# Performance work log

Measured on AMD Instinct MI355X. Metric: run time of the kernel, lower is better.

Reference implementation:

```python
import jax, jax.numpy as jnp
import numpy as np

B, T, D_IN, H, C = 16, 8192, 4, 256, 11


def setup_inputs() -> dict:
    key = jax.random.key(0)
    ks = jax.random.split(key, 9)
    sequence = jax.random.normal(ks[0], (B, T, D_IN), jnp.float32)
    # lengths in [7*T/8, T] so every sequence has mask[:,0]=True (torchcrf requirement)
    lengths = (T - jax.random.randint(ks[1], (B,), 0, T // 8)).astype(jnp.int64)
    labels = jax.random.randint(ks[2], (B, T), 0, C).astype(jnp.int64)
    W_enc = jax.random.normal(ks[3], (D_IN, H), jnp.float32) / np.float32(np.sqrt(D_IN))
    b_enc = jnp.zeros((H,), jnp.float32)
    W_emit = jax.random.normal(ks[4], (H, C), jnp.float32) / np.float32(np.sqrt(H))
    b_emit = jnp.zeros((C,), jnp.float32)
    start_trans = jax.random.normal(ks[5], (C,), jnp.float32) * 0.1
    trans = jax.random.normal(ks[6], (C, C), jnp.float32) * 0.1
    end_trans = jax.random.normal(ks[7], (C,), jnp.float32) * 0.1
    return dict(sequence=sequence, W_enc=W_enc, b_enc=b_enc, W_emit=W_emit,
                b_emit=b_emit, start_trans=start_trans, trans=trans,
                end_trans=end_trans, lengths=lengths, labels=labels)


def reference(sequence, W_enc, b_enc, W_emit, b_emit, start_trans, trans, end_trans, lengths, labels):
    # encoder (Linear + ReLU) and emission projection
    hidden = jax.nn.relu(sequence @ W_enc + b_enc)        # [B,T,H]
    em = hidden @ W_emit + b_emit                          # [B,T,C]
    mask = jnp.arange(T)[None, :] < lengths[:, None]       # [B,T] bool
    maskf = mask.astype(em.dtype)
    tags = jnp.where(labels == -100, 0, labels)            # -100 -> 0 as in compute_loss

    # ---- numerator: score of the gold path (torchcrf _compute_score) ----
    em_tag = jnp.take_along_axis(em, tags[..., None], axis=2)[..., 0]   # [B,T]
    trans_tag = trans[tags[:, :-1], tags[:, 1:]]                        # [B,T-1]
    num = start_trans[tags[:, 0]] + em_tag[:, 0]
    num = num + jnp.sum(maskf[:, 1:] * (trans_tag + em_tag[:, 1:]), axis=1)
    last_tag = tags[jnp.arange(B), lengths - 1]
    num = num + end_trans[last_tag]

    # ---- denominator: log partition via forward algorithm (torchcrf _compute_normalizer) ----
    alpha0 = start_trans[None, :] + em[:, 0]               # [B,C]
    em_rest = jnp.swapaxes(em[:, 1:], 0, 1)                # [T-1,B,C]
    mask_rest = jnp.swapaxes(mask[:, 1:], 0, 1)            # [T-1,B]

    def step(alpha, inp):
        em_t, m_t = inp
        nxt = jax.nn.logsumexp(alpha[:, :, None] + trans[None] + em_t[:, None, :], axis=1)
        return jnp.where(m_t[:, None], nxt, alpha), None

    alpha, _ = jax.lax.scan(step, alpha0, (em_rest, mask_rest))
    den = jax.nn.logsumexp(alpha + end_trans[None, :], axis=1)  # [B]

    # reduction='mean' over batch, loss = -log_likelihood
    return -jnp.mean(num - den)
```

## Files before the change

kernel.cpp:

```cpp
#include <hip/hip_runtime.h>
#include <hip/hip_bf16.h>

#define B_   16
#define T_   8192
#define H_   256
#define C_   11
#define KCH  256
#define LCH  32
#define NC   (B_*KCH)

typedef __attribute__((ext_vector_type(8))) short short8;
typedef __attribute__((ext_vector_type(4))) float f32x4;

__global__ __launch_bounds__(256) void k_em(
    const float* __restrict__ seq, const float* __restrict__ Wenc,
    const float* __restrict__ benc, const float* __restrict__ Wemit,
    const float* __restrict__ bemit, const float* __restrict__ trans,
    const float* __restrict__ startt, const float* __restrict__ endt,
    const int* __restrict__ lengths, const int* __restrict__ labels,
    unsigned short* __restrict__ expem, float* __restrict__ numpart,
    unsigned* __restrict__ counter)
{
    __shared__ float ldsWpack[2048];
    __shared__ float ldsWemit[4096];
    __shared__ float red[4];
    int tid = threadIdx.x;
    if (blockIdx.x == 0 && tid == 0) counter[0] = 0;

    for (int idx = tid; idx < 2048; idx += 256) {
        int h = idx >> 3, s = idx & 7;
        float v = 0.f;
        if (s < 4) v = Wenc[s * H_ + h];
        else if (s == 4) v = benc[h];
        ldsWpack[idx] = v;
    }
    for (int idx = tid; idx < 4096; idx += 256) {
        int h = idx >> 4, c = idx & 15;
        ldsWemit[idx] = (c < C_) ? Wemit[h * C_ + c] : 0.f;
    }
    __syncthreads();

    int wid = tid >> 6, lane = tid & 63;
    int g = lane >> 4, li = lane & 15;
    int b0 = blockIdx.x >> 5;
    int tb0 = (blockIdx.x & 31) * 256 + wid * 64;
    size_t grow0 = (size_t)b0 * T_ + tb0;

    float4 xs[4];
#pragma unroll
    for (int tt = 0; tt < 4; tt++)
        xs[tt] = *(const float4*)(seq + (grow0 + tt * 16 + li) * 4);

    f32x4 acc[4];
#pragma unroll
    for (int tt = 0; tt < 4; tt++) acc[tt] = (f32x4){0.f, 0.f, 0.f, 0.f};

#pragma unroll 1
    for (int kb = 0; kb < 8; kb++) {
        float We[8][5], wm[8];
#pragma unroll
        for (int e = 0; e < 8; e++) {
            int h = 32 * kb + 4 * g + (e & 3) + 16 * (e >> 2);
            float4 w4 = *(const float4*)&ldsWpack[h * 8];
            We[e][0] = w4.x; We[e][1] = w4.y; We[e][2] = w4.z; We[e][3] = w4.w;
            We[e][4] = ldsWpack[h * 8 + 4];
            wm[e] = ldsWemit[h * 16 + li];
        }
        unsigned a0, a1, a2, a3;
        asm("v_cvt_pk_bf16_f32 %0, %1, %2" : "=v"(a0) : "v"(wm[0]), "v"(wm[1]));
        asm("v_cvt_pk_bf16_f32 %0, %1, %2" : "=v"(a1) : "v"(wm[2]), "v"(wm[3]));
        asm("v_cvt_pk_bf16_f32 %0, %1, %2" : "=v"(a2) : "v"(wm[4]), "v"(wm[5]));
        asm("v_cvt_pk_bf16_f32 %0, %1, %2" : "=v"(a3) : "v"(wm[6]), "v"(wm[7]));
        union { short8 s8; uint4 u4; } au;
        au.u4 = make_uint4(a0, a1, a2, a3);

#pragma unroll
        for (int tt = 0; tt < 4; tt++) {
            float4 x = xs[tt];
            float hv[8];
#pragma unroll
            for (int e = 0; e < 8; e++) {
                float h = fmaf(x.x, We[e][0],
                          fmaf(x.y, We[e][1],
                          fmaf(x.z, We[e][2],
                          fmaf(x.w, We[e][3], We[e][4]))));
                hv[e] = fmaxf(h, 0.f);
            }
            unsigned u0, u1, u2, u3;
            asm("v_cvt_pk_bf16_f32 %0, %1, %2" : "=v"(u0) : "v"(hv[0]), "v"(hv[1]));
            asm("v_cvt_pk_bf16_f32 %0, %1, %2" : "=v"(u1) : "v"(hv[2]), "v"(hv[3]));
            asm("v_cvt_pk_bf16_f32 %0, %1, %2" : "=v"(u2) : "v"(hv[4]), "v"(hv[5]));
            asm("v_cvt_pk_bf16_f32 %0, %1, %2" : "=v"(u3) : "v"(hv[6]), "v"(hv[7]));
            union { short8 s8; uint4 u4; } bfu;
            bfu.u4 = make_uint4(u0, u1, u2, u3);
            acc[tt] = __builtin_amdgcn_mfma_f32_16x16x32_bf16(au.s8, bfu.s8, acc[tt], 0, 0, 0);
        }
    }

    int len = lengths[b0];
    const int* lab = labels + (size_t)b0 * T_;
    float bm[4];
#pragma unroll
    for (int r = 0; r < 4; r++) {
        int c = 4 * g + r;
        bm[r] = (c < C_) ? bemit[c] : 0.f;
    }

    float nacc = 0.f;
#pragma unroll
    for (int tt = 0; tt < 4; tt++) {
        float em0 = acc[tt].x + bm[0];
        float em1 = acc[tt].y + bm[1];
        float em2 = acc[tt].z + bm[2];
        float em3 = acc[tt].w + bm[3];

        int t = tb0 + tt * 16 + li;
        int tg = lab[t]; tg = tg < 0 ? 0 : tg;
        if (g == (tg >> 2) && t < len) {
            int r = tg & 3;
            float emtg = r == 0 ? em0 : r == 1 ? em1 : r == 2 ? em2 : em3;
            float contrib;
            if (t == 0) {
                contrib = startt[tg] + emtg;
            } else {
                int tp = lab[t - 1]; tp = tp < 0 ? 0 : tp;
                contrib = trans[tp * C_ + tg] + emtg;
            }
            if (t == len - 1) contrib += endt[tg];
            nacc += contrib;
        }

        if (g < 3) {
            float e0 = __expf(em0), e1 = __expf(em1);
            float e2 = __expf(em2), e3 = __expf(em3);
            unsigned u0, u1;
            asm("v_cvt_pk_bf16_f32 %0, %1, %2" : "=v"(u0) : "v"(e0), "v"(e1));
            asm("v_cvt_pk_bf16_f32 %0, %1, %2" : "=v"(u1) : "v"(e2), "v"(e3));
            *(uint2*)(expem + (grow0 + tt * 16 + li) * 16 + g * 4) = make_uint2(u0, u1);
        }
    }

#pragma unroll
    for (int off = 32; off > 0; off >>= 1) nacc += __shfl_down(nacc, off);
    if (lane == 0) red[wid] = nacc;
    __syncthreads();
    if (tid == 0) numpart[blockIdx.x] = red[0] + red[1] + red[2] + red[3];
}

__global__ __launch_bounds__(256) void k_chunks(
    const float* __restrict__ trans, const int* __restrict__ lengths,
    const unsigned short* __restrict__ expem, float* __restrict__ G)
{
    int tid = threadIdx.x;
    int wave = tid >> 6, lane = tid & 63;
    int i = lane & 15, g = lane >> 4;
    int cid = (blockIdx.x << 2) | wave;
    int b = cid >> 8, k = cid & (KCH - 1);
    int t0 = 1 + k * LCH;
    int len = lengths[b];
    bool writer = (i < C_) && (g < 3);
    float* o = G + (size_t)cid * 132 + i * 12 + 4 * g;

    if (t0 >= len) {
        if (writer) {
            float4 v;
            v.x = (4 * g + 0 == i) ? 1.f : 0.f;
            v.y = (4 * g + 1 == i) ? 1.f : 0.f;
            v.z = (4 * g + 2 == i) ? 1.f : 0.f;
            v.w = (g == 2) ? 0.f : ((4 * g + 3 == i) ? 1.f : 0.f);
            *(float4*)o = v;
        }
        return;
    }

    const unsigned short* emp = expem + ((size_t)b * T_ + t0) * 16 + 4 * g;

    uint2 Ld[4], Nd[4];
#pragma unroll
    for (int q = 0; q < 4; q++)
        Ld[q] = *(const uint2*)(emp + (size_t)q * 16);

    float af[4];
#pragma unroll
    for (int e = 0; e < 4; e++) {
        int kk = 4 * g + e;
        af[e] = (i < C_ && kk < C_) ? __expf(trans[kk * C_ + i]) : 0.f;
    }
    unsigned a0, a1;
    asm("v_cvt_pk_bf16_f32 %0, %1, %2" : "=v"(a0) : "v"(af[0]), "v"(af[1]));
    asm("v_cvt_pk_bf16_f32 %0, %1, %2" : "=v"(a1) : "v"(af[2]), "v"(af[3]));
    union { short8 s8; uint4 u4; } A; A.u4 = make_uint4(a0, a1, 0u, 0u);

    float p0 = (4 * g + 0 == i) ? 1.f : 0.f;
    float p1 = (4 * g + 1 == i) ? 1.f : 0.f;
    float p2 = (4 * g + 2 == i) ? 1.f : 0.f;
    float p3 = (4 * g + 3 == i) ? 1.f : 0.f;
    float ls = 0.f;

    int tl = t0 + LCH; if (len < tl) tl = len;

#pragma unroll 1
    for (int su = 0; su < LCH / 4; su++) {
        if (su < LCH / 4 - 1) {
#pragma unroll
            for (int q = 0; q < 4; q++)
                Nd[q] = *(const uint2*)(emp + (size_t)((su + 1) * 4 + q) * 16);
        }
#pragma unroll
        for (int ss = 0; ss < 4; ss++) {
            int t = t0 + su * 4 + ss;
            if (t < tl) {
                unsigned b0u, b1u;
                asm("v_cvt_pk_bf16_f32 %0, %1, %2" : "=v"(b0u) : "v"(p0), "v"(p1));
                asm("v_cvt_pk_bf16_f32 %0, %1, %2" : "=v"(b1u) : "v"(p2), "v"(p3));
                union { short8 s8; uint4 u4; } Bf; Bf.u4 = make_uint4(b0u, b1u, 0u, 0u);
                f32x4 acc = __builtin_amdgcn_mfma_f32_16x16x32_bf16(
                    A.s8, Bf.s8, (f32x4){0.f, 0.f, 0.f, 0.f}, 0, 0, 0);
                uint2 emu = Ld[ss];
                p0 = acc.x * __uint_as_float(emu.x << 16);
                p1 = acc.y * __uint_as_float(emu.x & 0xffff0000u);
                p2 = acc.z * __uint_as_float(emu.y << 16);
                p3 = acc.w * __uint_as_float(emu.y & 0xffff0000u);
            }
        }
        float part = (p0 + p1) + (p2 + p3);
        part += __shfl_xor(part, 16);
        part += __shfl_xor(part, 32);
        float r = 1.f / part;
        p0 *= r; p1 *= r; p2 *= r; p3 *= r;
        ls += __logf(part);
        if (su < LCH / 4 - 1) {
#pragma unroll
            for (int q = 0; q < 4; q++) Ld[q] = Nd[q];
        }
    }

    if (writer) {
        float w3 = (g == 2) ? ls : p3;
        *(float4*)o = make_float4(p0, p1, p2, w3);
    }
}

__global__ __launch_bounds__(512, 1) void k_comb(
    const float* __restrict__ startt, const float* __restrict__ endt,
    const unsigned short* __restrict__ expem, const float* __restrict__ G0,
    const float* __restrict__ numpart, float* __restrict__ dens,
    unsigned* __restrict__ counter, float* __restrict__ out)
{
    __shared__ float M[KCH * 132];
    int b = blockIdx.x, tid = threadIdx.x;

    float numb = 0.f;
    if (tid < 64) {
        float v = (tid < 32) ? numpart[b * 32 + tid] : 0.f;
#pragma unroll
        for (int off = 32; off > 0; off >>= 1) v += __shfl_down(v, off);
        numb = v;
    }

    const float4* src = (const float4*)(G0 + (size_t)b * KCH * 132);
    float4* dst = (float4*)M;
#pragma unroll 4
    for (int idx = tid; idx < KCH * 132 / 4; idx += 512) dst[idx] = src[idx];
    __syncthreads();

    for (int stride = 1; stride < KCH; stride <<= 1) {
        int npair = KCH / (2 * stride);
        for (int task = tid; task < npair * C_; task += 512) {
            int p = task / C_, i = task - p * C_;
            float* A  = M + (size_t)(2 * stride * p) * 132;
            float* Bm = M + (size_t)(2 * stride * p + stride) * 132;
            float a[C_];
#pragma unroll
            for (int kk = 0; kk < C_; kk++) a[kk] = A[i * 12 + kk];
            float als = A[i * 12 + 11];
            float m = Bm[11];
#pragma unroll
            for (int kk = 1; kk < C_; kk++) m = fmaxf(m, Bm[kk * 12 + 11]);
            float wv[C_];
#pragma unroll
            for (int kk = 0; kk < C_; kk++)
                wv[kk] = a[kk] * __expf(Bm[kk * 12 + 11] - m);
            float outv[C_];
#pragma unroll
            for (int j = 0; j < C_; j++) outv[j] = wv[0] * Bm[j];
#pragma unroll
            for (int kk = 1; kk < C_; kk++)
#pragma unroll
                for (int j = 0; j < C_; j++)
                    outv[j] = fmaf(wv[kk], Bm[kk * 12 + j], outv[j]);
            float s = 0.f;
#pragma unroll
            for (int j = 0; j < C_; j++) s += outv[j];
            float rr = 1.f / s;
#pragma unroll
            for (int j = 0; j < C_; j++) A[i * 12 + j] = outv[j] * rr;
            A[i * 12 + 11] = als + m + __logf(s);
        }
        __syncthreads();
    }

    if (tid == 0) {
        const float* Cm = M;
        const unsigned short* em0 = expem + (size_t)b * T_ * 16;
        float av[C_];
        float mm = -1e30f;
#pragma unroll
        for (int i2 = 0; i2 < C_; i2++) {
            float e0 = __uint_as_float((unsigned)em0[i2] << 16);
            av[i2] = startt[i2] + __logf(e0) + Cm[i2 * 12 + 11];
            mm = fmaxf(mm, av[i2]);
        }
        float S[C_];
#pragma unroll
        for (int j = 0; j < C_; j++) S[j] = 0.f;
#pragma unroll
        for (int i2 = 0; i2 < C_; i2++) {
            float e = __expf(av[i2] - mm);
#pragma unroll
            for (int j = 0; j < C_; j++) S[j] = fmaf(e, Cm[i2 * 12 + j], S[j]);
        }
        float tot = 0.f;
#pragma unroll
        for (int j = 0; j < C_; j++) tot += S[j] * __expf(endt[j]);
        float den = __logf(tot) + mm;

        float loss = numb - den;
        __hip_atomic_store(&dens[b], loss, __ATOMIC_RELEASE, __HIP_MEMORY_SCOPE_AGENT);
        unsigned old = __hip_atomic_fetch_add(counter, 1u, __ATOMIC_ACQ_REL,
                                              __HIP_MEMORY_SCOPE_AGENT);
        if (old == B_ - 1) {
            float s = 0.f;
#pragma unroll
            for (int j = 0; j < B_; j++)
                s += __hip_atomic_load(&dens[j], __ATOMIC_ACQUIRE,
                                       __HIP_MEMORY_SCOPE_AGENT);
            out[0] = -s / (float)B_;
        }
    }
}

extern "C" void kernel_launch(void* const* d_in, const int* in_sizes, int n_in,
                              void* d_out, int out_size, void* d_ws, size_t ws_size,
                              hipStream_t stream) {
    const float* seq    = (const float*)d_in[0];
    const float* Wenc   = (const float*)d_in[1];
    const float* benc   = (const float*)d_in[2];
    const float* Wemit  = (const float*)d_in[3];
    const float* bemit  = (const float*)d_in[4];
    const float* startt = (const float*)d_in[5];
    const float* trans  = (const float*)d_in[6];
    const float* endt   = (const float*)d_in[7];
    const int*   lengths= (const int*)d_in[8];
    const int*   labels = (const int*)d_in[9];

    char* w = (char*)d_ws;
    unsigned short* expem  = (unsigned short*)w;
    float*          G0     = (float*)(w + 4194304);
    float*          numpart= (float*)(w + 6356992);
    float*          dens   = (float*)(w + 6359040);
    unsigned*       counter= (unsigned*)(w + 6359104);
    float*          out    = (float*)d_out;

    k_em<<<512, 256, 0, stream>>>(seq, Wenc, benc, Wemit, bemit, trans,
                                  startt, endt, lengths, labels,
                                  expem, numpart, counter);
    k_chunks<<<1024, 256, 0, stream>>>(trans, lengths, expem, G0);
    k_comb<<<B_, 512, 0, stream>>>(startt, endt, expem, G0, numpart,
                                   dens, counter, out);
}
```

Measured before the change: 47.01 us.

## Pre-combine four chunk matrices per block in LDS before global tree reduction

Each k_chunks block now combines its four waves' chunk transfer matrices in shared memory with two levels of the log-scaled matrix product, writing one matrix per block instead of four. This cuts the G buffer to 64 matrices per sequence, so k_comb loads less and runs two fewer serial tree levels on only 16 blocks. The chunk loop is fully unrolled with all 32 emission rows preloaded, and the early-exit path for chunks past the sequence end is removed because masked chunks now yield identity via nact. The trade is extra syncthreads, more registers per k_chunks block, and idle waves during the in-block combine.

Result: faster. 45.23 us (-3.8%).

```diff
diff --git a/kernel.cpp b/kernel.cpp
--- a/kernel.cpp
+++ b/kernel.cpp
@@ -7,7 +7,7 @@
 #define C_   11
 #define KCH  256
 #define LCH  32
-#define NC   (B_*KCH)
+#define KL   64
 
 typedef __attribute__((ext_vector_type(8))) short short8;
 typedef __attribute__((ext_vector_type(4))) float f32x4;
@@ -147,38 +147,61 @@
     if (tid == 0) numpart[blockIdx.x] = red[0] + red[1] + red[2] + red[3];
 }
 
-__global__ __launch_bounds__(256) void k_chunks(
+__device__ __forceinline__ void combineRow(const float* __restrict__ A,
+                                           const float* __restrict__ Bm,
+                                           float* __restrict__ D, int i)
+{
+    float a[C_];
+#pragma unroll
+    for (int kk = 0; kk < C_; kk++) a[kk] = A[i * 12 + kk];
+    float als = A[i * 12 + 11];
+    float m = Bm[11];
+#pragma unroll
+    for (int kk = 1; kk < C_; kk++) m = fmaxf(m, Bm[kk * 12 + 11]);
+    float wv[C_];
+#pragma unroll
+    for (int kk = 0; kk < C_; kk++)
+        wv[kk] = a[kk] * __expf(Bm[kk * 12 + 11] - m);
+    float outv[C_];
+#pragma unroll
+    for (int j = 0; j < C_; j++) outv[j] = wv[0] * Bm[j];
+#pragma unroll
+    for (int kk = 1; kk < C_; kk++)
+#pragma unroll
+        for (int j = 0; j < C_; j++)
+            outv[j] = fmaf(wv[kk], Bm[kk * 12 + j], outv[j]);
+    float s = 0.f;
+#pragma unroll
+    for (int j = 0; j < C_; j++) s += outv[j];
+    float rr = 1.f / s;
+#pragma unroll
+    for (int j = 0; j < C_; j++) D[i * 12 + j] = outv[j] * rr;
+    D[i * 12 + 11] = als + m + __logf(s);
+}
+
+__global__ __launch_bounds__(256, 4) void k_chunks(
     const float* __restrict__ trans, const int* __restrict__ lengths,
     const unsigned short* __restrict__ expem, float* __restrict__ G)
 {
+    __shared__ float Mb[4][192];
     int tid = threadIdx.x;
     int wave = tid >> 6, lane = tid & 63;
     int i = lane & 15, g = lane >> 4;
-    int cid = (blockIdx.x << 2) | wave;
-    int b = cid >> 8, k = cid & (KCH - 1);
+
+    int bk = blockIdx.x;
+    int b = bk >> 6;
+    int k = ((bk & 63) << 2) | wave;
     int t0 = 1 + k * LCH;
     int len = lengths[b];
-    bool writer = (i < C_) && (g < 3);
-    float* o = G + (size_t)cid * 132 + i * 12 + 4 * g;
-
-    if (t0 >= len) {
-        if (writer) {
-            float4 v;
-            v.x = (4 * g + 0 == i) ? 1.f : 0.f;
-            v.y = (4 * g + 1 == i) ? 1.f : 0.f;
-            v.z = (4 * g + 2 == i) ? 1.f : 0.f;
-            v.w = (g == 2) ? 0.f : ((4 * g + 3 == i) ? 1.f : 0.f);
-            *(float4*)o = v;
-        }
-        return;
-    }
+    int tl = t0 + LCH; if (len < tl) tl = len;
+    int nact = tl - t0;
 
     const unsigned short* emp = expem + ((size_t)b * T_ + t0) * 16 + 4 * g;
 
-    uint2 Ld[4], Nd[4];
-#pragma unroll
-    for (int q = 0; q < 4; q++)
-        Ld[q] = *(const uint2*)(emp + (size_t)q * 16);
+    uint2 R[8][4];
+#pragma unroll
+    for (int q = 0; q < 16; q++)
+        R[q >> 2][q & 3] = *(const uint2*)(emp + (size_t)q * 16);
 
     float af[4];
 #pragma unroll
@@ -197,26 +220,23 @@
     float p3 = (4 * g + 3 == i) ? 1.f : 0.f;
     float ls = 0.f;
 
-    int tl = t0 + LCH; if (len < tl) tl = len;
-
-#pragma unroll 1
-    for (int su = 0; su < LCH / 4; su++) {
-        if (su < LCH / 4 - 1) {
+#pragma unroll
+    for (int su = 0; su < 8; su++) {
+        if (su < 4) {
 #pragma unroll
             for (int q = 0; q < 4; q++)
-                Nd[q] = *(const uint2*)(emp + (size_t)((su + 1) * 4 + q) * 16);
+                R[su + 4][q] = *(const uint2*)(emp + (size_t)((su + 4) * 4 + q) * 16);
         }
 #pragma unroll
         for (int ss = 0; ss < 4; ss++) {
-            int t = t0 + su * 4 + ss;
-            if (t < tl) {
+            if (su * 4 + ss < nact) {
                 unsigned b0u, b1u;
                 asm("v_cvt_pk_bf16_f32 %0, %1, %2" : "=v"(b0u) : "v"(p0), "v"(p1));
                 asm("v_cvt_pk_bf16_f32 %0, %1, %2" : "=v"(b1u) : "v"(p2), "v"(p3));
                 union { short8 s8; uint4 u4; } Bf; Bf.u4 = make_uint4(b0u, b1u, 0u, 0u);
                 f32x4 acc = __builtin_amdgcn_mfma_f32_16x16x32_bf16(
                     A.s8, Bf.s8, (f32x4){0.f, 0.f, 0.f, 0.f}, 0, 0, 0);
-                uint2 emu = Ld[ss];
+                uint2 emu = R[su][ss];
                 p0 = acc.x * __uint_as_float(emu.x << 16);
                 p1 = acc.y * __uint_as_float(emu.x & 0xffff0000u);
                 p2 = acc.z * __uint_as_float(emu.y << 16);
@@ -229,15 +249,53 @@
         float r = 1.f / part;
         p0 *= r; p1 *= r; p2 *= r; p3 *= r;
         ls += __logf(part);
-        if (su < LCH / 4 - 1) {
-#pragma unroll
-            for (int q = 0; q < 4; q++) Ld[q] = Nd[q];
-        }
-    }
-
-    if (writer) {
+    }
+
+    if (i < C_ && g < 3) {
         float w3 = (g == 2) ? ls : p3;
-        *(float4*)o = make_float4(p0, p1, p2, w3);
+        *(float4*)&Mb[wave][i * 12 + 4 * g] = make_float4(p0, p1, p2, w3);
+    }
+    __syncthreads();
+
+    if ((wave == 0 || wave == 2) && lane < C_)
+        combineRow(Mb[wave], Mb[wave + 1], Mb[wave], lane);
+    __syncthreads();
+
+    if (wave == 0 && lane < C_) {
+        float out[12];
+        {
+            const float* Aa = Mb[0]; const float* Bm = Mb[2];
+            float a[C_];
+#pragma unroll
+            for (int kk = 0; kk < C_; kk++) a[kk] = Aa[lane * 12 + kk];
+            float als = Aa[lane * 12 + 11];
+            float m = Bm[11];
+#pragma unroll
+            for (int kk = 1; kk < C_; kk++) m = fmaxf(m, Bm[kk * 12 + 11]);
+            float wv[C_];
+#pragma unroll
+            for (int kk = 0; kk < C_; kk++)
+                wv[kk] = a[kk] * __expf(Bm[kk * 12 + 11] - m);
+            float outv[C_];
+#pragma unroll
+            for (int j = 0; j < C_; j++) outv[j] = wv[0] * Bm[j];
+#pragma unroll
+            for (int kk = 1; kk < C_; kk++)
+#pragma unroll
+                for (int j = 0; j < C_; j++)
+                    outv[j] = fmaf(wv[kk], Bm[kk * 12 + j], outv[j]);
+            float s = 0.f;
+#pragma unroll
+            for (int j = 0; j < C_; j++) s += outv[j];
+            float rr = 1.f / s;
+#pragma unroll
+            for (int j = 0; j < C_; j++) out[j] = outv[j] * rr;
+            out[11] = als + m + __logf(s);
+        }
+        float* o = G + ((size_t)b * KL + (bk & 63)) * 132 + lane * 12;
+        *(float4*)(o + 0) = make_float4(out[0], out[1], out[2], out[3]);
+        *(float4*)(o + 4) = make_float4(out[4], out[5], out[6], out[7]);
+        *(float4*)(o + 8) = make_float4(out[8], out[9], out[10], out[11]);
     }
 }
 
@@ -247,7 +305,7 @@
     const float* __restrict__ numpart, float* __restrict__ dens,
     unsigned* __restrict__ counter, float* __restrict__ out)
 {
-    __shared__ float M[KCH * 132];
+    __shared__ float M[KL * 132];
     int b = blockIdx.x, tid = threadIdx.x;
 
     float numb = 0.f;
@@ -258,44 +316,19 @@
         numb = v;
     }
 
-    const float4* src = (const float4*)(G0 + (size_t)b * KCH * 132);
+    const float4* src = (const float4*)(G0 + (size_t)b * KL * 132);
     float4* dst = (float4*)M;
 #pragma unroll 4
-    for (int idx = tid; idx < KCH * 132 / 4; idx += 512) dst[idx] = src[idx];
+    for (int idx = tid; idx < KL * 132 / 4; idx += 512) dst[idx] = src[idx];
     __syncthreads();
 
-    for (int stride = 1; stride < KCH; stride <<= 1) {
-        int npair = KCH / (2 * stride);
+    for (int stride = 1; stride < KL; stride <<= 1) {
+        int npair = KL / (2 * stride);
         for (int task = tid; task < npair * C_; task += 512) {
             int p = task / C_, i = task - p * C_;
             float* A  = M + (size_t)(2 * stride * p) * 132;
             float* Bm = M + (size_t)(2 * stride * p + stride) * 132;
-            float a[C_];
-#pragma unroll
-            for (int kk = 0; kk < C_; kk++) a[kk] = A[i * 12 + kk];
-            float als = A[i * 12 + 11];
-            float m = Bm[11];
-#pragma unroll
-            for (int kk = 1; kk < C_; kk++) m = fmaxf(m, Bm[kk * 12 + 11]);
-            float wv[C_];
-#pragma unroll
-            for (int kk = 0; kk < C_; kk++)
-                wv[kk] = a[kk] * __expf(Bm[kk * 12 + 11] - m);
-            float outv[C_];
-#pragma unroll
-            for (int j = 0; j < C_; j++) outv[j] = wv[0] * Bm[j];
-#pragma unroll
-            for (int kk = 1; kk < C_; kk++)
-#pragma unroll
-                for (int j = 0; j < C_; j++)
-                    outv[j] = fmaf(wv[kk], Bm[kk * 12 + j], outv[j]);
-            float s = 0.f;
-#pragma unroll
-            for (int j = 0; j < C_; j++) s += outv[j];
-            float rr = 1.f / s;
-#pragma unroll
-            for (int j = 0; j < C_; j++) A[i * 12 + j] = outv[j] * rr;
-            A[i * 12 + 11] = als + m + __logf(s);
+            combineRow(A, Bm, A, i);
         }
         __syncthreads();
     }
@@ -357,9 +390,9 @@
     char* w = (char*)d_ws;
     unsigned short* expem  = (unsigned short*)w;
     float*          G0     = (float*)(w + 4194304);
-    float*          numpart= (float*)(w + 6356992);
-    float*          dens   = (float*)(w + 6359040);
-    unsigned*       counter= (unsigned*)(w + 6359104);
+    float*          numpart= (float*)(w + 4734976);
+    float*          dens   = (float*)(w + 4737024);
+    unsigned*       counter= (unsigned*)(w + 4737088);
     float*          out    = (float*)d_out;
 
     k_em<<<512, 256, 0, stream>>>(seq, Wenc, benc, Wemit, bemit, trans,
```
